# Kernel optimization log

Hardware: AMD Instinct MI355X
Metric: run time of the kernel (lower is better)

Reference implementation:

```python
import jax, jax.numpy as jnp
import numpy as np

HIDDEN = 4096       # in_features of gate/up proj
INTER = 11008       # intermediate_size (per projection)
GROUP = 128         # GPTQ group size
B, S = 4, 2048
NIB = jnp.uint32(0xF)


def _pack_rows(nib):
    """Pack 4-bit values along rows: [8*R, C] uint32 -> [R, C] uint32."""
    r = nib.reshape(-1, 8, nib.shape[-1])
    shifts = (jnp.arange(8, dtype=jnp.uint32) * 4)[None, :, None]
    return jnp.sum(r << shifts, axis=1, dtype=jnp.uint32)  # disjoint bits -> sum == OR


def _pack_cols(nib):
    """Pack 4-bit values along cols: [G, 8*C] uint32 -> [G, C] uint32."""
    r = nib.reshape(nib.shape[0], -1, 8)
    shifts = (jnp.arange(8, dtype=jnp.uint32) * 4)[None, None, :]
    return jnp.sum(r << shifts, axis=2, dtype=jnp.uint32)


def setup_inputs() -> dict:
    key = jax.random.key(0)
    ks = jax.random.split(key, 7)
    n_groups = HIDDEN // GROUP          # 32 groups for gate_up
    n_groups_d = INTER // GROUP         # 86 groups for down

    x = jax.random.normal(ks[0], (B, S, HIDDEN), jnp.float32)

    # gate_up_proj: in=HIDDEN, out=2*INTER
    nib_w_gu = jax.random.randint(ks[1], (HIDDEN, 2 * INTER), 0, 16).astype(jnp.uint32)
    nib_z_gu = jax.random.randint(ks[2], (n_groups, 2 * INTER), 0, 15).astype(jnp.uint32)
    qweight_gu = _pack_rows(nib_w_gu)                          # [HIDDEN//8, 2*INTER]
    qzeros_gu = _pack_cols(nib_z_gu)                           # [n_groups, 2*INTER//8]
    scales_gu = jax.random.uniform(ks[3], (n_groups, 2 * INTER), jnp.float32, 0.005, 0.02)
    g_idx_gu = (jnp.arange(HIDDEN, dtype=jnp.int32) // GROUP)

    # down_proj: in=INTER, out=HIDDEN
    nib_w_d = jax.random.randint(ks[4], (INTER, HIDDEN), 0, 16).astype(jnp.uint32)
    nib_z_d = jax.random.randint(ks[5], (n_groups_d, HIDDEN), 0, 15).astype(jnp.uint32)
    qweight_down = _pack_rows(nib_w_d)                         # [INTER//8, HIDDEN]
    qzeros_down = _pack_cols(nib_z_d)                          # [n_groups_d, HIDDEN//8]
    scales_down = jax.random.uniform(ks[6], (n_groups_d, HIDDEN), jnp.float32, 0.005, 0.02)
    g_idx_down = (jnp.arange(INTER, dtype=jnp.int32) // GROUP)

    return {
        "x": x,
        "qweight_gu": qweight_gu, "qzeros_gu": qzeros_gu,
        "scales_gu": scales_gu, "g_idx_gu": g_idx_gu,
        "qweight_down": qweight_down, "qzeros_down": qzeros_down,
        "scales_down": scales_down, "g_idx_down": g_idx_down,
    }


def _dequant(qw, qz, sc, g_idx):
    """GPTQ v2 dequant: W[i,j] = sc[g[i],j] * (wq[i,j] - (zq[g[i],j] + 1))."""
    shifts = jnp.arange(8, dtype=jnp.uint32) * 4
    # unpack qweight along rows: [R, C] -> [8*R, C]
    wq = ((qw[:, None, :] >> shifts[None, :, None]) & NIB)
    wq = wq.reshape(-1, qw.shape[1]).astype(jnp.float32)
    # unpack qzeros along cols: [G, C//8] -> [G, C]; +1 per GPTQ v2 convention
    zq = ((qz[:, :, None] >> shifts[None, None, :]) & NIB)
    zq = zq.reshape(qz.shape[0], -1).astype(jnp.float32) + 1.0
    return sc[g_idx] * (wq - zq[g_idx])  # [in, out]


def reference(x, qweight_gu, qzeros_gu, scales_gu, g_idx_gu,
              qweight_down, qzeros_down, scales_down, g_idx_down):
    w_gu = _dequant(qweight_gu, qzeros_gu, scales_gu, g_idx_gu)          # [HIDDEN, 2*INTER]
    inter = jnp.einsum('bsh,hf->bsf', x, w_gu)                            # [B,S,2*INTER]
    gate, up = inter[..., :INTER], inter[..., INTER:]
    h = jax.nn.silu(gate) * up                                            # SwiGLU
    w_d = _dequant(qweight_down, qzeros_down, scales_down, g_idx_down)   # [INTER, HIDDEN]
    return jnp.einsum('bsf,fh->bsh', h, w_d)
```

## Files before the change

### kernel.cpp

```cpp
#include <hip/hip_runtime.h>
#include <stdint.h>

#define HIDDEN 4096
#define INTER  11008
#define NTOK   8192

typedef __bf16 bf16;
typedef __bf16 bf16x8 __attribute__((ext_vector_type(8)));
typedef float  f32x4  __attribute__((ext_vector_type(4)));

__device__ __forceinline__ void gload16(const void* g, void* l) {
  __builtin_amdgcn_global_load_lds(
      (const __attribute__((address_space(1))) void*)g,
      (__attribute__((address_space(3))) void*)l, 16, 0, 0);
}

__global__ __launch_bounds__(256) void cvt_bf16_kernel(const float* __restrict__ x,
                                                       bf16* __restrict__ y) {
  const int i = (blockIdx.x * 256 + threadIdx.x) * 8;
  f32x4 a = *(const f32x4*)(x + i);
  f32x4 b = *(const f32x4*)(x + i + 4);
  bf16x8 v;
#pragma unroll
  for (int e = 0; e < 4; ++e) { v[e] = (bf16)a[e]; v[e + 4] = (bf16)b[e]; }
  *(bf16x8*)(y + i) = v;
}

template <bool ILV>
__global__ __launch_bounds__(256) void dequant_kernel(const uint32_t* __restrict__ qw,
                                                      const uint32_t* __restrict__ qz,
                                                      const float* __restrict__ sc,
                                                      bf16* __restrict__ out,
                                                      int J, int Kout) {
  __shared__ __align__(16) bf16 T[64 * 256];
  const int tid = threadIdx.x;
  const int tx = tid & 63, ty = tid >> 6;
  const int j0 = blockIdx.x * 64, r0 = blockIdx.y * 32;
  const int j = j0 + tx;
  const int J8 = J >> 3;
#pragma unroll
  for (int i = 0; i < 8; ++i) {
    const int r = r0 + ty * 8 + i;
    const int g = r >> 4;
    const uint32_t w = qw[(size_t)r * J + j];
    const float s = sc[(size_t)g * J + j];
    const uint32_t zb = (qz[(size_t)g * J8 + (j >> 3)] >> ((j & 7) * 4)) & 15u;
    const float zoff = (float)(zb + 1u);
    bf16x8 v;
#pragma unroll
    for (int e = 0; e < 8; ++e) {
      const float wv = (float)((w >> (e * 4)) & 15u);
      v[e] = (bf16)(s * (wv - zoff));
    }
    const int lb = (tx * 512 + (ty * 8 + i) * 16) ^ ((tx & 31) << 4);
    *(bf16x8*)((char*)T + lb) = v;
  }
  __syncthreads();
#pragma unroll
  for (int u = 0; u < 8; ++u) {
    const int unit = u * 256 + tid;
    const int jj = unit >> 5;
    const int ob = (unit & 31) * 16;
    const int lb = (jj * 512 + ob) ^ ((jj & 31) << 4);
    bf16x8 v = *(const bf16x8*)((const char*)T + lb);
    const int jg = j0 + jj;
    int rowm;
    if (ILV) {
      rowm = (jg < INTER) ? ((jg >> 4) * 32 + (jg & 15))
                          : (((jg - INTER) >> 4) * 32 + 16 + ((jg - INTER) & 15));
    } else {
      rowm = jg;
    }
    *(bf16x8*)(out + (size_t)rowm * Kout + r0 * 8 + (ob >> 1)) = v;
  }
}

#define OFF_A 0
#define OFF_B 32768

#define STG(mat, buf, h, t)                                                    \
  do {                                                                         \
    gload16(s##mat[h][0] + (size_t)(t) * 128,                                  \
            lds + (buf) * 65536 + OFF_##mat + (h) * 16384 + w * 1024);         \
    gload16(s##mat[h][1] + (size_t)(t) * 128,                                  \
            lds + (buf) * 65536 + OFF_##mat + (h) * 16384 + 8192 + w * 1024);  \
  } while (0)

#define BAR __builtin_amdgcn_s_barrier()
#define LGKM0                                              \
  do {                                                     \
    asm volatile("s_waitcnt lgkmcnt(0)" ::: "memory");     \
    __builtin_amdgcn_sched_barrier(0);                     \
  } while (0)
#define VM6 asm volatile("s_waitcnt vmcnt(6)" ::: "memory")

#define MFMA_Q(MH, NH)                                                         \
  do {                                                                         \
    __builtin_amdgcn_s_setprio(1);                                             \
    _Pragma("unroll") for (int mi = 0; mi < 4; ++mi) {                         \
      _Pragma("unroll") for (int nj = 0; nj < 2; ++nj) {                       \
        acc[(MH)*4 + mi][(NH)*2 + nj] = __builtin_amdgcn_mfma_f32_16x16x32_bf16( \
            av[mi][0], bv[nj][0], acc[(MH)*4 + mi][(NH)*2 + nj], 0, 0, 0);     \
        acc[(MH)*4 + mi][(NH)*2 + nj] = __builtin_amdgcn_mfma_f32_16x16x32_bf16( \
            av[mi][1], bv[nj][1], acc[(MH)*4 + mi][(NH)*2 + nj], 0, 0, 0);     \
      }                                                                        \
    }                                                                          \
    __builtin_amdgcn_s_setprio(0);                                             \
    __builtin_amdgcn_sched_barrier(0);                                         \
  } while (0)

template <int K, int NT, int NNB, bool FUSED>
__global__ __launch_bounds__(512, 2) void gemm8p(const bf16* __restrict__ A,
                                                 const bf16* __restrict__ Bm,
                                                 void* __restrict__ Cout) {
  extern __shared__ char lds[];
  const int tid = threadIdx.x;
  const int lane = tid & 63, w = tid >> 6;
  const int wr = w >> 2, wc = w & 3;
  const int fr = lane & 15, fg = lane >> 4;

  const int wg = blockIdx.x;
  const int nb = wg % NNB, mb = wg / NNB;
  const int m0 = mb << 8, n0 = nb << 8;

  const char* sA[2][2];
  const char* sB[2][2];
#pragma unroll
  for (int h = 0; h < 2; ++h)
#pragma unroll
    for (int l = 0; l < 2; ++l) {
      const int d = h * 16384 + (l * 512 + tid) * 16;
      const int r = d >> 7;
      const int c2 = d & 127;
      const int cL = c2 ^ ((r & 7) << 4);
      sA[h][l] = (const char*)A + (size_t)(m0 + r) * (size_t)(K * 2) + cL;
      sB[h][l] = (const char*)Bm + (size_t)(n0 + r) * (size_t)(K * 2) + cL;
    }

  const int swz = (fr & 7) << 4;
  const int ck[2] = {(fg * 16) ^ swz, (64 + fg * 16) ^ swz};
  const int aro = (wr * 64 + fr) * 128;
  const int bro = OFF_B + (wc * 32 + fr) * 128;

  auto lda = [&](int buf, int mh, int mi, int kk) -> bf16x8 {
    return *(const bf16x8*)(lds + buf * 65536 + mh * 16384 + aro + mi * 2048 + ck[kk]);
  };
  auto ldb = [&](int buf, int nh, int nj, int kk) -> bf16x8 {
    return *(const bf16x8*)(lds + buf * 65536 + bro + nh * 16384 + nj * 2048 + ck[kk]);
  };

  f32x4 acc[8][4];
#pragma unroll
  for (int i = 0; i < 8; ++i)
#pragma unroll
    for (int j = 0; j < 4; ++j) acc[i][j] = (f32x4)0.0f;
  bf16x8 av[4][2], bv[2][2];

  STG(B, 0, 0, 0);
  STG(A, 0, 0, 0);
  STG(B, 0, 1, 0);
  STG(A, 0, 1, 0);
  STG(A, 1, 0, 1);
  STG(B, 1, 1, 1);
  STG(A, 1, 1, 1);
  VM6;
  BAR;

  for (int t = 0; t < NT; ++t) {
    const int cb = t & 1, nx = cb ^ 1;
    const int t1 = (t + 1 < NT) ? t + 1 : 0;
    const int t2 = (t + 2 < NT) ? t + 2 : 0;

#pragma unroll
    for (int mi = 0; mi < 4; ++mi) { av[mi][0] = lda(cb, 0, mi, 0); av[mi][1] = lda(cb, 0, mi, 1); }
#pragma unroll
    for (int nj = 0; nj < 2; ++nj) { bv[nj][0] = ldb(cb, 0, nj, 0); bv[nj][1] = ldb(cb, 0, nj, 1); }
    STG(B, nx, 0, t1);
    BAR; LGKM0;
    MFMA_Q(0, 0);
    BAR;

#pragma unroll
    for (int nj = 0; nj < 2; ++nj) { bv[nj][0] = ldb(cb, 1, nj, 0); bv[nj][1] = ldb(cb, 1, nj, 1); }
    STG(A, cb, 0, t2);
    BAR; LGKM0;
    MFMA_Q(0, 1);
    BAR;

#pragma unroll
    for (int mi = 0; mi < 4; ++mi) { av[mi][0] = lda(cb, 1, mi, 0); av[mi][1] = lda(cb, 1, mi, 1); }
    STG(B, cb, 1, t2);
    BAR; LGKM0;
    MFMA_Q(1, 1);
    BAR;

#pragma unroll
    for (int nj = 0; nj < 2; ++nj) { bv[nj][0] = ldb(cb, 0, nj, 0); bv[nj][1] = ldb(cb, 0, nj, 1); }
    STG(A, cb, 1, t2);
    VM6;
    BAR; LGKM0;
    MFMA_Q(1, 0);
    BAR;
  }

  if constexpr (FUSED) {
    bf16* H = (bf16*)Cout;
#pragma unroll
    for (int mh = 0; mh < 2; ++mh)
#pragma unroll
      for (int mi = 0; mi < 4; ++mi)
#pragma unroll
        for (int nh = 0; nh < 2; ++nh) {
          const f32x4 g = acc[mh * 4 + mi][nh * 2];
          const f32x4 u = acc[mh * 4 + mi][nh * 2 + 1];
          const int col = (n0 >> 1) + wc * 16 + nh * 64 + fr;
#pragma unroll
          for (int rr = 0; rr < 4; ++rr) {
            const int row = m0 + wr * 64 + mh * 128 + mi * 16 + fg * 4 + rr;
            const float gv = g[rr], uv = u[rr];
            H[(size_t)row * INTER + col] = (bf16)(gv / (1.0f + __expf(-gv)) * uv);
          }
        }
  } else {
    float* O = (float*)Cout;
#pragma unroll
    for (int mh = 0; mh < 2; ++mh)
#pragma unroll
      for (int mi = 0; mi < 4; ++mi)
#pragma unroll
        for (int nh = 0; nh < 2; ++nh)
#pragma unroll
          for (int nj = 0; nj < 2; ++nj) {
            const f32x4 a = acc[mh * 4 + mi][nh * 2 + nj];
            const int col = n0 + wc * 32 + nh * 128 + nj * 16 + fr;
#pragma unroll
            for (int rr = 0; rr < 4; ++rr) {
              const int row = m0 + wr * 64 + mh * 128 + mi * 16 + fg * 4 + rr;
              __builtin_nontemporal_store(a[rr], &O[(size_t)row * HIDDEN + col]);
            }
          }
  }
}

extern "C" void kernel_launch(void* const* d_in, const int* in_sizes, int n_in,
                              void* d_out, int out_size, void* d_ws, size_t ws_size,
                              hipStream_t stream) {
  (void)in_sizes; (void)n_in; (void)out_size; (void)ws_size;
  const float*    x     = (const float*)d_in[0];
  const uint32_t* qw_gu = (const uint32_t*)d_in[1];
  const uint32_t* qz_gu = (const uint32_t*)d_in[2];
  const float*    sc_gu = (const float*)d_in[3];
  const uint32_t* qw_d  = (const uint32_t*)d_in[5];
  const uint32_t* qz_d  = (const uint32_t*)d_in[6];
  const float*    sc_d  = (const float*)d_in[7];
  float*          out   = (float*)d_out;

  char* ws = (char*)d_ws;
  const size_t XB = (size_t)NTOK * HIDDEN * 2;
  const size_t WT = (size_t)2 * INTER * HIDDEN * 2;
  bf16* xb = (bf16*)ws;
  bf16* wt = (bf16*)(ws + XB);
  bf16* hb = (bf16*)(ws + XB + WT);

  hipFuncSetAttribute((const void*)&gemm8p<HIDDEN, HIDDEN / 64, 2 * INTER / 256, true>,
                      hipFuncAttributeMaxDynamicSharedMemorySize, 131072);
  hipFuncSetAttribute((const void*)&gemm8p<INTER, INTER / 64, HIDDEN / 256, false>,
                      hipFuncAttributeMaxDynamicSharedMemorySize, 131072);

  cvt_bf16_kernel<<<NTOK * HIDDEN / 2048, 256, 0, stream>>>(x, xb);

  dequant_kernel<true><<<dim3((2 * INTER) / 64, (HIDDEN / 8) / 32), 256, 0, stream>>>(
      qw_gu, qz_gu, sc_gu, wt, 2 * INTER, HIDDEN);
  gemm8p<HIDDEN, HIDDEN / 64, 2 * INTER / 256, true>
      <<<(2 * INTER / 256) * (NTOK / 256), 512, 131072, stream>>>(xb, wt, hb);

  dequant_kernel<false><<<dim3(HIDDEN / 64, (INTER / 8) / 32), 256, 0, stream>>>(
      qw_d, qz_d, sc_d, wt, HIDDEN, INTER);
  gemm8p<INTER, INTER / 64, HIDDEN / 256, false>
      <<<(HIDDEN / 256) * (NTOK / 256), 512, 131072, stream>>>(hb, wt, out);
}
```

Before: 2.015 ms.

## Fuse int4 dequant into gate/up GEMM using fp16 magic-number unpack

Replaces the separate gate_up dequant pass plus bf16 GEMM with a GEMM that streams packed int4 weights into LDS and unpacks them in registers via the 0x6400 fp16 magic-number trick. A small pre-kernel packs each group's scale and zero+1024 into fp16 pairs, and x is converted to fp16 instead of bf16. This removes the write and re-read of the ~180MB dequantized gate_up matrix. In exchange it adds VALU unpack work inside the MFMA loop and changes numerics to fp16 for activations and weights.

Measured after the change: 2.294 ms. +13.8%, slower.

```diff
diff --git a/kernel.cpp b/kernel.cpp
--- a/kernel.cpp
+++ b/kernel.cpp
@@ -4,9 +4,13 @@
 #define HIDDEN 4096
 #define INTER  11008
 #define NTOK   8192
+#define WROW   22016
 
 typedef __bf16 bf16;
 typedef __bf16 bf16x8 __attribute__((ext_vector_type(8)));
+typedef _Float16 f16;
+typedef _Float16 f16x2 __attribute__((ext_vector_type(2)));
+typedef _Float16 f16x8 __attribute__((ext_vector_type(8)));
 typedef float  f32x4  __attribute__((ext_vector_type(4)));
 
 __device__ __forceinline__ void gload16(const void* g, void* l) {
@@ -14,19 +18,40 @@
       (const __attribute__((address_space(1))) void*)g,
       (__attribute__((address_space(3))) void*)l, 16, 0, 0);
 }
-
-__global__ __launch_bounds__(256) void cvt_bf16_kernel(const float* __restrict__ x,
-                                                       bf16* __restrict__ y) {
+__device__ __forceinline__ void gload4(const void* g, void* l) {
+  __builtin_amdgcn_global_load_lds(
+      (const __attribute__((address_space(1))) void*)g,
+      (__attribute__((address_space(3))) void*)l, 4, 0, 0);
+}
+
+__global__ __launch_bounds__(256) void cvt_f16_kernel(const float* __restrict__ x,
+                                                      f16* __restrict__ y) {
   const int i = (blockIdx.x * 256 + threadIdx.x) * 8;
   f32x4 a = *(const f32x4*)(x + i);
   f32x4 b = *(const f32x4*)(x + i + 4);
-  bf16x8 v;
-#pragma unroll
-  for (int e = 0; e < 4; ++e) { v[e] = (bf16)a[e]; v[e + 4] = (bf16)b[e]; }
-  *(bf16x8*)(y + i) = v;
-}
-
-template <bool ILV>
+  f16x8 v;
+#pragma unroll
+  for (int e = 0; e < 4; ++e) { v[e] = (f16)a[e]; v[e + 4] = (f16)b[e]; }
+  *(f16x8*)(y + i) = v;
+}
+
+__global__ __launch_bounds__(256) void spak_kernel(const uint32_t* __restrict__ qz,
+                                                   const float* __restrict__ sc,
+                                                   uint32_t* __restrict__ outp) {
+  const int idx = blockIdx.x * 256 + threadIdx.x;
+  const int gq = idx / WROW;
+  const int n = idx - gq * WROW;
+  const int grp = n >> 5, win = n & 31;
+  const int jg = (win < 16) ? grp * 16 + win : INTER + grp * 16 + (win - 16);
+  const float s = sc[(size_t)gq * WROW + jg];
+  const uint32_t z = (qz[(size_t)gq * (WROW / 8) + (jg >> 3)] >> ((jg & 7) * 4)) & 15u;
+  union { f16 h[2]; uint32_t u; } a, b;
+  a.h[0] = (f16)s; a.h[1] = (f16)s;
+  b.h[0] = (f16)(float)(1025u + z); b.h[1] = b.h[0];
+  outp[(size_t)idx * 2 + 0] = a.u;
+  outp[(size_t)idx * 2 + 1] = b.u;
+}
+
 __global__ __launch_bounds__(256) void dequant_kernel(const uint32_t* __restrict__ qw,
                                                       const uint32_t* __restrict__ qz,
                                                       const float* __restrict__ sc,
@@ -63,38 +88,225 @@
     const int ob = (unit & 31) * 16;
     const int lb = (jj * 512 + ob) ^ ((jj & 31) << 4);
     bf16x8 v = *(const bf16x8*)((const char*)T + lb);
-    const int jg = j0 + jj;
-    int rowm;
-    if (ILV) {
-      rowm = (jg < INTER) ? ((jg >> 4) * 32 + (jg & 15))
-                          : (((jg - INTER) >> 4) * 32 + 16 + ((jg - INTER) & 15));
-    } else {
-      rowm = jg;
+    *(bf16x8*)(out + (size_t)(j0 + jj) * Kout + r0 * 8 + (ob >> 1)) = v;
+  }
+}
+
+#define OFF_BP 65536
+#define OFF_SPK 82176
+
+#define BAR __builtin_amdgcn_s_barrier()
+#define LGKM0                                              \
+  do {                                                     \
+    asm volatile("s_waitcnt lgkmcnt(0)" ::: "memory");     \
+    __builtin_amdgcn_sched_barrier(0);                     \
+  } while (0)
+#define VM2 asm volatile("s_waitcnt vmcnt(2)" ::: "memory")
+
+#define STG_A(buf, h, tt)                                                     \
+  do {                                                                        \
+    gload16(sA[h][0] + (size_t)(tt) * 128,                                    \
+            lds + (buf) * 32768 + (h) * 16384 + w * 1024);                    \
+    gload16(sA[h][1] + (size_t)(tt) * 128,                                    \
+            lds + (buf) * 32768 + (h) * 16384 + 8192 + w * 1024);             \
+  } while (0)
+
+#define STG_B(buf, tt)                                                        \
+  gload16(bsrc + (size_t)(8 * (tt) + w) * WROW,                               \
+          lds + OFF_BP + (buf) * 8320 + w * 1040)
+
+#define STG_SPK(gt)                                                           \
+  gload4(spakg + ((size_t)(gt) * WROW + n0) * 2 + tid,                        \
+         lds + OFF_SPK + ((gt) & 3) * 2048 + w * 256)
+
+#define MFMA_Q(MH, NH)                                                         \
+  do {                                                                         \
+    __builtin_amdgcn_s_setprio(1);                                             \
+    _Pragma("unroll") for (int mi = 0; mi < 4; ++mi) {                         \
+      _Pragma("unroll") for (int nj = 0; nj < 2; ++nj) {                       \
+        acc[(MH)*4 + mi][(NH)*2 + nj] = __builtin_amdgcn_mfma_f32_16x16x32_f16( \
+            av[mi][0], bv[nj][0], acc[(MH)*4 + mi][(NH)*2 + nj], 0, 0, 0);     \
+        acc[(MH)*4 + mi][(NH)*2 + nj] = __builtin_amdgcn_mfma_f32_16x16x32_f16( \
+            av[mi][1], bv[nj][1], acc[(MH)*4 + mi][(NH)*2 + nj], 0, 0, 0);     \
+      }                                                                        \
+    }                                                                          \
+    __builtin_amdgcn_s_setprio(0);                                             \
+    __builtin_amdgcn_sched_barrier(0);                                         \
+  } while (0)
+
+__device__ __forceinline__ f16x8 unpack8(uint32_t u, f16x2 s2, f16x2 k2) {
+  const uint32_t M = 0x64006400u;
+  uint32_t q0 = (u & 0xFu)         | ((u << 12) & 0xF0000u) | M;
+  uint32_t q1 = ((u >> 8) & 0xFu)  | ((u << 4)  & 0xF0000u) | M;
+  uint32_t q2 = ((u >> 16) & 0xFu) | ((u >> 4)  & 0xF0000u) | M;
+  uint32_t q3 = ((u >> 24) & 0xFu) | ((u >> 12) & 0xF0000u) | M;
+  f16x2 w0 = (__builtin_bit_cast(f16x2, q0) - k2) * s2;
+  f16x2 w1 = (__builtin_bit_cast(f16x2, q1) - k2) * s2;
+  f16x2 w2 = (__builtin_bit_cast(f16x2, q2) - k2) * s2;
+  f16x2 w3 = (__builtin_bit_cast(f16x2, q3) - k2) * s2;
+  f16x8 r;
+  r[0] = w0[0]; r[1] = w0[1]; r[2] = w1[0]; r[3] = w1[1];
+  r[4] = w2[0]; r[5] = w2[1]; r[6] = w3[0]; r[7] = w3[1];
+  return r;
+}
+
+__global__ __launch_bounds__(512, 2) void gemm1q(const f16* __restrict__ A,
+                                                 const uint32_t* __restrict__ qw,
+                                                 const uint32_t* __restrict__ spakg,
+                                                 bf16* __restrict__ H) {
+  extern __shared__ char lds[];
+  const int tid = threadIdx.x;
+  const int lane = tid & 63, w = tid >> 6;
+  const int wr = w >> 2, wc = w & 3;
+  const int fr = lane & 15, fg = lane >> 4;
+  constexpr int NT = HIDDEN / 64;
+
+  const int wg = blockIdx.x;
+  const int nb = wg % (WROW / 256), mb = wg / (WROW / 256);
+  const int m0 = mb << 8, n0 = nb << 8;
+
+  const char* sA[2][2];
+#pragma unroll
+  for (int h = 0; h < 2; ++h)
+#pragma unroll
+    for (int l = 0; l < 2; ++l) {
+      const int d = h * 16384 + (l * 512 + tid) * 16;
+      const int r = d >> 7;
+      const int cL = (d & 127) ^ ((r & 7) << 4);
+      sA[h][l] = (const char*)A + (size_t)(m0 + r) * (size_t)(HIDDEN * 2) + cL;
     }
-    *(bf16x8*)(out + (size_t)rowm * Kout + r0 * 8 + (ob >> 1)) = v;
+  const int n4 = n0 + lane * 4;
+  const int grp4 = n4 >> 5, win4 = n4 & 31;
+  const int jg4 = (win4 < 16) ? grp4 * 16 + win4 : INTER + grp4 * 16 + (win4 - 16);
+  const uint32_t* bsrc = qw + jg4;
+
+  const int swz = (fr & 7) << 4;
+  const int ck[2] = {(fg * 16) ^ swz, (64 + fg * 16) ^ swz};
+  const int aro = (wr * 64 + fr) * 128;
+  auto lda = [&](int buf, int mh, int mi, int kk) -> f16x8 {
+    return *(const f16x8*)(lds + buf * 32768 + mh * 16384 + aro + mi * 2048 + ck[kk]);
+  };
+  const int ncol[2][2] = {{wc * 32 + fr, wc * 32 + 16 + fr},
+                          {wc * 32 + 128 + fr, wc * 32 + 144 + fr}};
+
+  f32x4 acc[8][4];
+#pragma unroll
+  for (int i = 0; i < 8; ++i)
+#pragma unroll
+    for (int j = 0; j < 4; ++j) acc[i][j] = (f32x4)0.0f;
+  f16x8 av[4][2], bv[2][2];
+  f16x2 s2r[2][2], k2r[2][2];
+
+  STG_A(0, 0, 0);
+  STG_A(0, 1, 0);
+  STG_B(0, 0);
+  STG_SPK(0);
+  STG_SPK(1);
+  STG_A(1, 1, 1);
+  VM2;
+  BAR;
+
+  for (int t = 0; t < NT; ++t) {
+    const int cb = t & 1, nx = cb ^ 1, g = t >> 1;
+    const int t1 = (t + 1 < NT) ? t + 1 : 0;
+    const int t2 = (t + 2 < NT) ? t + 2 : 0;
+
+#pragma unroll
+    for (int mi = 0; mi < 4; ++mi) { av[mi][0] = lda(cb, 0, mi, 0); av[mi][1] = lda(cb, 0, mi, 1); }
+    uint32_t bu[2][2];
+#pragma unroll
+    for (int nj = 0; nj < 2; ++nj)
+#pragma unroll
+      for (int kk = 0; kk < 2; ++kk)
+        bu[nj][kk] = *(const uint32_t*)(lds + OFF_BP + cb * 8320 + (kk * 4 + fg) * 1040 +
+                                        ncol[0][nj] * 4);
+    if ((t & 1) == 0) {
+      const char* sp = lds + OFF_SPK + (g & 3) * 2048;
+#pragma unroll
+      for (int nh = 0; nh < 2; ++nh)
+#pragma unroll
+        for (int nj = 0; nj < 2; ++nj) {
+          s2r[nh][nj] = *(const f16x2*)(sp + ncol[nh][nj] * 8);
+          k2r[nh][nj] = *(const f16x2*)(sp + ncol[nh][nj] * 8 + 4);
+        }
+    }
+    STG_A(nx, 0, t1);
+    STG_B(nx, t1);
+    BAR; LGKM0;
+#pragma unroll
+    for (int nj = 0; nj < 2; ++nj)
+#pragma unroll
+      for (int kk = 0; kk < 2; ++kk)
+        bv[nj][kk] = unpack8(bu[nj][kk], s2r[0][nj], k2r[0][nj]);
+    MFMA_Q(0, 0);
+    BAR;
+
+#pragma unroll
+    for (int mi = 0; mi < 4; ++mi) { av[mi][0] = lda(cb, 1, mi, 0); av[mi][1] = lda(cb, 1, mi, 1); }
+    BAR; LGKM0;
+    MFMA_Q(1, 0);
+    BAR;
+
+#pragma unroll
+    for (int nj = 0; nj < 2; ++nj)
+#pragma unroll
+      for (int kk = 0; kk < 2; ++kk)
+        bu[nj][kk] = *(const uint32_t*)(lds + OFF_BP + cb * 8320 + (kk * 4 + fg) * 1040 +
+                                        ncol[1][nj] * 4);
+    STG_A(cb, 1, t2);
+    BAR; LGKM0;
+#pragma unroll
+    for (int nj = 0; nj < 2; ++nj)
+#pragma unroll
+      for (int kk = 0; kk < 2; ++kk)
+        bv[nj][kk] = unpack8(bu[nj][kk], s2r[1][nj], k2r[1][nj]);
+    MFMA_Q(1, 1);
+    BAR;
+
+#pragma unroll
+    for (int mi = 0; mi < 4; ++mi) { av[mi][0] = lda(cb, 0, mi, 0); av[mi][1] = lda(cb, 0, mi, 1); }
+    VM2;
+    if ((t & 1) == 0) {
+      const int gt = (g + 2 < 32) ? g + 2 : 31;
+      STG_SPK(gt);
+    }
+    BAR; LGKM0;
+    MFMA_Q(0, 1);
+    BAR;
   }
-}
-
-#define OFF_A 0
-#define OFF_B 32768
-
-#define STG(mat, buf, h, t)                                                    \
+  asm volatile("s_waitcnt vmcnt(0)" ::: "memory");
+
+#pragma unroll
+  for (int mh = 0; mh < 2; ++mh)
+#pragma unroll
+    for (int mi = 0; mi < 4; ++mi)
+#pragma unroll
+      for (int nh = 0; nh < 2; ++nh) {
+        const f32x4 gv4 = acc[mh * 4 + mi][nh * 2];
+        const f32x4 uv4 = acc[mh * 4 + mi][nh * 2 + 1];
+        const int col = (n0 >> 1) + wc * 16 + nh * 64 + fr;
+#pragma unroll
+        for (int rr = 0; rr < 4; ++rr) {
+          const int row = m0 + wr * 64 + mh * 128 + mi * 16 + fg * 4 + rr;
+          const float gv = gv4[rr], uv = uv4[rr];
+          H[(size_t)row * INTER + col] = (bf16)(gv / (1.0f + __expf(-gv)) * uv);
+        }
+      }
+}
+
+#define OFF_A2 0
+#define OFF_B2 32768
+
+#define STG2(mat, buf, h, t)                                                   \
   do {                                                                         \
     gload16(s##mat[h][0] + (size_t)(t) * 128,                                  \
             lds + (buf) * 65536 + OFF_##mat + (h) * 16384 + w * 1024);         \
     gload16(s##mat[h][1] + (size_t)(t) * 128,                                  \
             lds + (buf) * 65536 + OFF_##mat + (h) * 16384 + 8192 + w * 1024);  \
   } while (0)
-
-#define BAR __builtin_amdgcn_s_barrier()
-#define LGKM0                                              \
-  do {                                                     \
-    asm volatile("s_waitcnt lgkmcnt(0)" ::: "memory");     \
-    __builtin_amdgcn_sched_barrier(0);                     \
-  } while (0)
 #define VM6 asm volatile("s_waitcnt vmcnt(6)" ::: "memory")
 
-#define MFMA_Q(MH, NH)                                                         \
+#define MFMA_Q2(MH, NH)                                                        \
   do {                                                                         \
     __builtin_amdgcn_s_setprio(1);                                             \
     _Pragma("unroll") for (int mi = 0; mi < 4; ++mi) {                         \
@@ -109,10 +321,10 @@
     __builtin_amdgcn_sched_barrier(0);                                         \
   } while (0)
 
-template <int K, int NT, int NNB, bool FUSED>
+template <int K, int NT, int NNB>
 __global__ __launch_bounds__(512, 2) void gemm8p(const bf16* __restrict__ A,
                                                  const bf16* __restrict__ Bm,
-                                                 void* __restrict__ Cout) {
+                                                 float* __restrict__ O) {
   extern __shared__ char lds[];
   const int tid = threadIdx.x;
   const int lane = tid & 63, w = tid >> 6;
@@ -123,24 +335,23 @@
   const int nb = wg % NNB, mb = wg / NNB;
   const int m0 = mb << 8, n0 = nb << 8;
 
-  const char* sA[2][2];
-  const char* sB[2][2];
+  const char* sA2[2][2];
+  const char* sB2[2][2];
 #pragma unroll
   for (int h = 0; h < 2; ++h)
 #pragma unroll
     for (int l = 0; l < 2; ++l) {
       const int d = h * 16384 + (l * 512 + tid) * 16;
       const int r = d >> 7;
-      const int c2 = d & 127;
-      const int cL = c2 ^ ((r & 7) << 4);
-      sA[h][l] = (const char*)A + (size_t)(m0 + r) * (size_t)(K * 2) + cL;
-      sB[h][l] = (const char*)Bm + (size_t)(n0 + r) * (size_t)(K * 2) + cL;
+      const int cL = (d & 127) ^ ((r & 7) << 4);
+      sA2[h][l] = (const char*)A + (size_t)(m0 + r) * (size_t)(K * 2) + cL;
+      sB2[h][l] = (const char*)Bm + (size_t)(n0 + r) * (size_t)(K * 2) + cL;
     }
 
   const int swz = (fr & 7) << 4;
   const int ck[2] = {(fg * 16) ^ swz, (64 + fg * 16) ^ swz};
   const int aro = (wr * 64 + fr) * 128;
-  const int bro = OFF_B + (wc * 32 + fr) * 128;
+  const int bro = OFF_B2 + (wc * 32 + fr) * 128;
 
   auto lda = [&](int buf, int mh, int mi, int kk) -> bf16x8 {
     return *(const bf16x8*)(lds + buf * 65536 + mh * 16384 + aro + mi * 2048 + ck[kk]);
@@ -156,13 +367,13 @@
     for (int j = 0; j < 4; ++j) acc[i][j] = (f32x4)0.0f;
   bf16x8 av[4][2], bv[2][2];
 
-  STG(B, 0, 0, 0);
-  STG(A, 0, 0, 0);
-  STG(B, 0, 1, 0);
-  STG(A, 0, 1, 0);
-  STG(A, 1, 0, 1);
-  STG(B, 1, 1, 1);
-  STG(A, 1, 1, 1);
+  STG2(A2, 0, 0, 0);
+  STG2(B2, 0, 0, 0);
+  STG2(B2, 0, 1, 0);
+  STG2(A2, 0, 1, 0);
+  STG2(A2, 1, 0, 1);
+  STG2(B2, 1, 1, 1);
+  STG2(A2, 1, 1, 1);
   VM6;
   BAR;
 
@@ -175,71 +386,50 @@
     for (int mi = 0; mi < 4; ++mi) { av[mi][0] = lda(cb, 0, mi, 0); av[mi][1] = lda(cb, 0, mi, 1); }
 #pragma unroll
     for (int nj = 0; nj < 2; ++nj) { bv[nj][0] = ldb(cb, 0, nj, 0); bv[nj][1] = ldb(cb, 0, nj, 1); }
-    STG(B, nx, 0, t1);
-    BAR; LGKM0;
-    MFMA_Q(0, 0);
+    STG2(B2, nx, 0, t1);
+    BAR; LGKM0;
+    MFMA_Q2(0, 0);
     BAR;
 
 #pragma unroll
     for (int nj = 0; nj < 2; ++nj) { bv[nj][0] = ldb(cb, 1, nj, 0); bv[nj][1] = ldb(cb, 1, nj, 1); }
-    STG(A, cb, 0, t2);
-    BAR; LGKM0;
-    MFMA_Q(0, 1);
+    STG2(A2, cb, 0, t2);
+    BAR; LGKM0;
+    MFMA_Q2(0, 1);
     BAR;
 
 #pragma unroll
     for (int mi = 0; mi < 4; ++mi) { av[mi][0] = lda(cb, 1, mi, 0); av[mi][1] = lda(cb, 1, mi, 1); }
-    STG(B, cb, 1, t2);
-    BAR; LGKM0;
-    MFMA_Q(1, 1);
+    STG2(B2, cb, 1, t2);
+    BAR; LGKM0;
+    MFMA_Q2(1, 1);
     BAR;
 
 #pragma unroll
     for (int nj = 0; nj < 2; ++nj) { bv[nj][0] = ldb(cb, 0, nj, 0); bv[nj][1] = ldb(cb, 0, nj, 1); }
-    STG(A, cb, 1, t2);
+    STG2(A2, cb, 1, t2);
     VM6;
     BAR; LGKM0;
-    MFMA_Q(1, 0);
+    MFMA_Q2(1, 0);
     BAR;
   }
 
-  if constexpr (FUSED) {
-    bf16* H = (bf16*)Cout;
-#pragma unroll
-    for (int mh = 0; mh < 2; ++mh)
-#pragma unroll
-      for (int mi = 0; mi < 4; ++mi)
-#pragma unroll
-        for (int nh = 0; nh < 2; ++nh) {
-          const f32x4 g = acc[mh * 4 + mi][nh * 2];
-          const f32x4 u = acc[mh * 4 + mi][nh * 2 + 1];
-          const int col = (n0 >> 1) + wc * 16 + nh * 64 + fr;
+#pragma unroll
+  for (int mh = 0; mh < 2; ++mh)
+#pragma unroll
+    for (int mi = 0; mi < 4; ++mi)
+#pragma unroll
+      for (int nh = 0; nh < 2; ++nh)
+#pragma unroll
+        for (int nj = 0; nj < 2; ++nj) {
+          const f32x4 a = acc[mh * 4 + mi][nh * 2 + nj];
+          const int col = n0 + wc * 32 + nh * 128 + nj * 16 + fr;
 #pragma unroll
           for (int rr = 0; rr < 4; ++rr) {
             const int row = m0 + wr * 64 + mh * 128 + mi * 16 + fg * 4 + rr;
-            const float gv = g[rr], uv = u[rr];
-            H[(size_t)row * INTER + col] = (bf16)(gv / (1.0f + __expf(-gv)) * uv);
+            __builtin_nontemporal_store(a[rr], &O[(size_t)row * HIDDEN + col]);
           }
         }
-  } else {
-    float* O = (float*)Cout;
-#pragma unroll
-    for (int mh = 0; mh < 2; ++mh)
-#pragma unroll
-      for (int mi = 0; mi < 4; ++mi)
-#pragma unroll
-        for (int nh = 0; nh < 2; ++nh)
-#pragma unroll
-          for (int nj = 0; nj < 2; ++nj) {
-            const f32x4 a = acc[mh * 4 + mi][nh * 2 + nj];
-            const int col = n0 + wc * 32 + nh * 128 + nj * 16 + fr;
-#pragma unroll
-            for (int rr = 0; rr < 4; ++rr) {
-              const int row = m0 + wr * 64 + mh * 128 + mi * 16 + fg * 4 + rr;
-              __builtin_nontemporal_store(a[rr], &O[(size_t)row * HIDDEN + col]);
-            }
-          }
-  }
 }
 
 extern "C" void kernel_launch(void* const* d_in, const int* in_sizes, int n_in,
@@ -256,26 +446,26 @@
   float*          out   = (float*)d_out;
 
   char* ws = (char*)d_ws;
-  const size_t XB = (size_t)NTOK * HIDDEN * 2;
-  const size_t WT = (size_t)2 * INTER * HIDDEN * 2;
-  bf16* xb = (bf16*)ws;
-  bf16* wt = (bf16*)(ws + XB);
-  bf16* hb = (bf16*)(ws + XB + WT);
-
-  hipFuncSetAttribute((const void*)&gemm8p<HIDDEN, HIDDEN / 64, 2 * INTER / 256, true>,
+  const size_t XB  = (size_t)NTOK * HIDDEN * 2;
+  const size_t W2B = (size_t)HIDDEN * INTER * 2;
+  const size_t HB  = (size_t)NTOK * INTER * 2;
+  f16*      xb    = (f16*)ws;
+  bf16*     wt    = (bf16*)(ws + XB);
+  bf16*     hb    = (bf16*)(ws + XB + W2B);
+  uint32_t* spakg = (uint32_t*)(ws + XB + W2B + HB);
+
+  hipFuncSetAttribute((const void*)&gemm1q,
+                      hipFuncAttributeMaxDynamicSharedMemorySize, 90368);
+  hipFuncSetAttribute((const void*)&gemm8p<INTER, INTER / 64, HIDDEN / 256>,
                       hipFuncAttributeMaxDynamicSharedMemorySize, 131072);
-  hipFuncSetAttribute((const void*)&gemm8p<INTER, INTER / 64, HIDDEN / 256, false>,
-                      hipFuncAttributeMaxDynamicSharedMemorySize, 131072);
-
-  cvt_bf16_kernel<<<NTOK * HIDDEN / 2048, 256, 0, stream>>>(x, xb);
-
-  dequant_kernel<true><<<dim3((2 * INTER) / 64, (HIDDEN / 8) / 32), 256, 0, stream>>>(
-      qw_gu, qz_gu, sc_gu, wt, 2 * INTER, HIDDEN);
-  gemm8p<HIDDEN, HIDDEN / 64, 2 * INTER / 256, true>
-      <<<(2 * INTER / 256) * (NTOK / 256), 512, 131072, stream>>>(xb, wt, hb);
-
-  dequant_kernel<false><<<dim3(HIDDEN / 64, (INTER / 8) / 32), 256, 0, stream>>>(
+
+  cvt_f16_kernel<<<NTOK * HIDDEN / 2048, 256, 0, stream>>>(x, xb);
+  spak_kernel<<<32 * WROW / 256, 256, 0, stream>>>(qz_gu, sc_gu, spakg);
+
+  gemm1q<<<(WROW / 256) * (NTOK / 256), 512, 90368, stream>>>(xb, qw_gu, spakg, hb);
+
+  dequant_kernel<<<dim3(HIDDEN / 64, (INTER / 8) / 32), 256, 0, stream>>>(
       qw_d, qz_d, sc_d, wt, HIDDEN, INTER);
-  gemm8p<INTER, INTER / 64, HIDDEN / 256, false>
+  gemm8p<INTER, INTER / 64, HIDDEN / 256>
       <<<(HIDDEN / 256) * (NTOK / 256), 512, 131072, stream>>>(hb, wt, out);
 }
```
